# Optimization experiments

Hardware: AMD Instinct MI355X
Metric: run time of the kernel (lower is better)

## Reference

```python
import jax, jax.numpy as jnp
import numpy as np


def setup_inputs() -> dict:
    key = jax.random.key(0)
    k1, k2, k3, k4, k5 = jax.random.split(key, 5)
    B, T, H, E, F = 4, 2048, 2048, 8, 1024
    s_h = 1.0 / np.sqrt(H)
    s_f = 1.0 / np.sqrt(F)
    return {
        "hidden_states": jax.random.normal(k1, (B, T, H), dtype=jnp.float32),
        "W_router": jax.random.normal(k2, (H, E), dtype=jnp.float32) * s_h,
        "W_gate": jax.random.normal(k3, (E, H, F), dtype=jnp.float32) * s_h,
        "W_up": jax.random.normal(k4, (E, H, F), dtype=jnp.float32) * s_h,
        "W_down": jax.random.normal(k5, (E, F, H), dtype=jnp.float32) * s_f,
    }


def reference(hidden_states, W_router, W_gate, W_up, W_down):
    B, T, H = hidden_states.shape
    E = W_router.shape[1]
    x = hidden_states.reshape(-1, H)  # [N, H]
    # ReMoE router: linear -> ReLU, non-negative weights per expert
    weights = jax.nn.relu(x @ W_router)  # [N, E]
    # Per-expert SwiGLU FFN applied to all tokens; zero-weight experts
    # contribute exactly zero, matching the original masked dispatch.
    gate = jnp.einsum('nh,ehf->enf', x, W_gate)  # [E, N, F]
    up = jnp.einsum('nh,ehf->enf', x, W_up)      # [E, N, F]
    hid = jax.nn.silu(gate) * up                 # [E, N, F]
    expert_out = jnp.einsum('enf,efh->enh', hid, W_down)  # [E, N, H]
    out_flat = jnp.einsum('ne,enh->nh', weights, expert_out)  # [N, H]
    out = out_flat.reshape(B, T, H)
    router_weights = weights.reshape(B, T, E)
    return (out, router_weights)
```

## Files before the change

kernel.cpp:

```cpp
#include <hip/hip_runtime.h>
#include <hip/hip_bf16.h>

#define N_TOK 8192
#define HD    2048
#define NE    8
#define FF    1024

using f32x4  = __attribute__((ext_vector_type(4))) float;
using bf16x8 = __attribute__((ext_vector_type(8))) __bf16;

__device__ __forceinline__ unsigned short f2bf(float f) {
  unsigned u = __float_as_uint(f);
  u += 0x7FFFu + ((u >> 16) & 1u);
  return (unsigned short)(u >> 16);
}

__device__ __forceinline__ void gl_lds16(const void* g, void* l) {
  __builtin_amdgcn_global_load_lds((__attribute__((address_space(1))) void*)g,
                                   (__attribute__((address_space(3))) void*)l,
                                   16, 0, 0);
}

__device__ __forceinline__ void stage256(const unsigned short* g, size_t lda, int k0,
                                         char* slotbase, int wv, int sr8, int scol) {
  #pragma unroll
  for (int c = 0; c < 4; ++c) {
    const int grp = c * 8 + wv;
    gl_lds16(g + (size_t)(grp * 8 + sr8) * lda + k0 + scol, slotbase + grp * 1024);
  }
}
__device__ __forceinline__ void stage256i(const unsigned short* const aP[4], int k0,
                                          char* slotbase, int wv) {
  #pragma unroll
  for (int c = 0; c < 4; ++c) {
    const int grp = c * 8 + wv;
    gl_lds16(aP[c] + k0, slotbase + grp * 1024);
  }
}
__device__ __forceinline__ void stage128(const unsigned short* g, size_t lda, int k0,
                                         char* slotbase, int wv, int sr8, int scol) {
  #pragma unroll
  for (int c = 0; c < 2; ++c) {
    const int grp = c * 8 + wv;
    gl_lds16(g + (size_t)(grp * 8 + sr8) * lda + k0 + scol, slotbase + grp * 1024);
  }
}

__global__ void k_tconv(const float* __restrict__ in, unsigned short* __restrict__ out,
                        int R, int C, size_t in_z, size_t out_z, size_t ostride) {
  __shared__ float tile[32][33];
  const int z = blockIdx.z;
  const int c0 = blockIdx.x * 32, r0 = blockIdx.y * 32;
  const int tx = threadIdx.x, ty = threadIdx.y;
  const float* ip = in + (size_t)z * in_z;
  unsigned short* op = out + (size_t)z * out_z;
  #pragma unroll
  for (int i = ty; i < 32; i += 8)
    tile[i][tx] = ip[(size_t)(r0 + i) * C + (c0 + tx)];
  __syncthreads();
  #pragma unroll
  for (int i = ty; i < 32; i += 8)
    op[(size_t)(c0 + i) * ostride + (r0 + tx)] = f2bf(tile[tx][i]);
}

__global__ void k_router(const float* __restrict__ x, const float* __restrict__ Wr,
                         float* __restrict__ w, float* __restrict__ rout,
                         unsigned short* __restrict__ xb) {
  const int lane = threadIdx.x & 63, wv = threadIdx.x >> 6;
  const int n = blockIdx.x * 4 + wv;
  const float* xr = x + (size_t)n * HD + lane * 32;
  unsigned short* xbr = xb + (size_t)n * HD + lane * 32;
  const float* wbase = Wr + (size_t)lane * 32 * NE;
  float acc[8];
  #pragma unroll
  for (int e = 0; e < 8; ++e) acc[e] = 0.f;
  #pragma unroll
  for (int kk = 0; kk < 32; kk += 4) {
    float4 xv = *reinterpret_cast<const float4*>(xr + kk);
    ushort4 o;
    o.x = f2bf(xv.x); o.y = f2bf(xv.y); o.z = f2bf(xv.z); o.w = f2bf(xv.w);
    *reinterpret_cast<ushort4*>(xbr + kk) = o;
    #pragma unroll
    for (int t = 0; t < 4; ++t) {
      const float* wrow = wbase + (kk + t) * 8;
      float4 w0 = *reinterpret_cast<const float4*>(wrow);
      float4 w1 = *reinterpret_cast<const float4*>(wrow + 4);
      float xs = (t == 0) ? xv.x : (t == 1) ? xv.y : (t == 2) ? xv.z : xv.w;
      acc[0] += xs * w0.x; acc[1] += xs * w0.y; acc[2] += xs * w0.z; acc[3] += xs * w0.w;
      acc[4] += xs * w1.x; acc[5] += xs * w1.y; acc[6] += xs * w1.z; acc[7] += xs * w1.w;
    }
  }
  #pragma unroll
  for (int off = 32; off; off >>= 1) {
    #pragma unroll
    for (int e = 0; e < 8; ++e) acc[e] += __shfl_down(acc[e], off);
  }
  if (lane == 0) {
    #pragma unroll
    for (int e = 0; e < 8; ++e) {
      float v = acc[e] > 0.f ? acc[e] : 0.f;
      w[n * 8 + e] = v;
      rout[n * 8 + e] = v;
    }
  }
}

__global__ void k_compact(const float* __restrict__ w, int* __restrict__ idx,
                          int* __restrict__ rev, int* __restrict__ cnt) {
  const int e = blockIdx.x;
  __shared__ int base;
  __shared__ int scan[4];
  if (threadIdx.x == 0) base = 0;
  __syncthreads();
  const int lane = threadIdx.x & 63, wvi = threadIdx.x >> 6;
  for (int c0 = 0; c0 < N_TOK; c0 += 256) {
    const int n = c0 + threadIdx.x;
    const bool act = w[n * 8 + e] > 0.f;
    unsigned long long m = __ballot(act);
    const int pre  = __popcll(m & ((1ull << lane) - 1ull));
    if (lane == 0) scan[wvi] = __popcll(m);
    __syncthreads();
    int woff = 0;
    #pragma unroll
    for (int i = 0; i < 4; ++i) if (i < wvi) woff += scan[i];
    const int tot = scan[0] + scan[1] + scan[2] + scan[3];
    const int pos = base + woff + pre;
    if (act) idx[e * N_TOK + pos] = n;
    rev[n * NE + e] = act ? pos : -1;
    __syncthreads();
    if (threadIdx.x == 0) base += tot;
    __syncthreads();
  }
  const int M = base;
  if (threadIdx.x == 0) cnt[e] = M;
  const int Mpad = (M + 255) & ~255;
  for (int i = M + threadIdx.x; i < Mpad; i += 256) idx[e * N_TOK + i] = 0;
}

#define G1_PHASE(cpK) do {                                                       \
    const char* Ab_ = As + rs * 32768 + (wr * 64) * 128 + rb;                    \
    const char* Bg_ = Bgs + rs * 16384 + (wc * 64) * 128 + rb;                   \
    const char* Bu_ = Bus + rs * 16384 + (wc * 64) * 128 + rb;                   \
    bf16x8 av_[4], bg_[4], bu_[4];                                               \
    _Pragma("unroll")                                                            \
    for (int i = 0; i < 4; ++i) av_[i] = *(const bf16x8*)(Ab_ + i * 2048 + (cpK)); \
    _Pragma("unroll")                                                            \
    for (int j = 0; j < 4; ++j) {                                                \
      bg_[j] = *(const bf16x8*)(Bg_ + j * 2048 + (cpK));                         \
      bu_[j] = *(const bf16x8*)(Bu_ + j * 2048 + (cpK));                         \
    }                                                                            \
    __builtin_amdgcn_s_setprio(1);                                               \
    _Pragma("unroll")                                                            \
    for (int i = 0; i < 4; ++i) {                                                \
      _Pragma("unroll")                                                          \
      for (int j = 0; j < 4; ++j) {                                              \
        ag[i][j] = __builtin_amdgcn_mfma_f32_16x16x32_bf16(av_[i], bg_[j], ag[i][j], 0,0,0); \
        au[i][j] = __builtin_amdgcn_mfma_f32_16x16x32_bf16(av_[i], bu_[j], au[i][j], 0,0,0); \
      }                                                                          \
    }                                                                            \
    __builtin_amdgcn_s_setprio(0);                                               \
  } while (0)

__global__ void __launch_bounds__(512, 2) k_gemm1(
    const unsigned short* __restrict__ xb,
    const unsigned short* __restrict__ Wg,
    const unsigned short* __restrict__ Wu,
    const float* __restrict__ w,
    const int* __restrict__ idx,
    const int* __restrict__ cnt,
    unsigned short* __restrict__ A2,
    int e0, int k2g, int nwg, int compacted) {
  extern __shared__ char lds[];
  char* As  = lds;
  char* Bgs = lds + 65536;
  char* Bus = lds + 98304;
  const int tid = threadIdx.x;
  const int l = tid & 63, wv = tid >> 6;

  const int h = blockIdx.x;
  const int chunk = nwg >> 3;
  const int L = (h & 7) * chunk + (h >> 3);
  const int eloc = L >> 8;
  const int e = e0 + eloc;
  const int idxq = L & 255;
  const int sub = idxq >> 5;
  const int f = ((sub & 1) << 2) | ((idxq >> 3) & 3);
  const int y = ((sub >> 1) << 3) | (idxq & 7);
  const int bm = y << 8;
  const int bf = f << 7;
  const int wr = wv >> 1, wc = wv & 1;

  const int Me = cnt[e];
  if (bm >= Me) return;
  const int* idxe = idx + e * N_TOK;

  const unsigned short* gBg = Wg + ((size_t)e * FF + bf) * HD;
  const unsigned short* gBu = Wu + ((size_t)e * FF + bf) * HD;

  const int sr8  = l >> 3;
  const int scol = ((l & 7) ^ sr8) << 3;
  const int fr  = l & 15;
  const int rb  = fr << 7;
  const int kc  = (l >> 4) << 4;
  const int swz = (l & 7) << 4;
  const int cp0 = kc ^ swz;
  const int cp1 = (64 + kc) ^ swz;

  const unsigned short* aP[4];
  #pragma unroll
  for (int c = 0; c < 4; ++c)
    aP[c] = xb + (size_t)idxe[bm + (c * 8 + wv) * 8 + sr8] * HD + scol;

  f32x4 ag[4][4], au[4][4];
  const f32x4 zero = {0.f, 0.f, 0.f, 0.f};
  #pragma unroll
  for (int i = 0; i < 4; ++i) {
    #pragma unroll
    for (int j = 0; j < 4; ++j) { ag[i][j] = zero; au[i][j] = zero; }
  }

  stage256i(aP, 0, As, wv);
  stage128(gBg, HD, 0, Bgs, wv, sr8, scol);
  stage128(gBu, HD, 0, Bus, wv, sr8, scol);
  asm volatile("s_waitcnt vmcnt(0)" ::: "memory");
  __builtin_amdgcn_s_barrier();
  __builtin_amdgcn_sched_barrier(0);

  const int NT = HD / 64;
  for (int t = 0; t < NT; ++t) {
    const int tn = (t + 1 < NT) ? t + 1 : NT - 1;
    const int sw = (t + 1) & 1;
    const int rs = t & 1;
    stage128(gBg, HD, tn * 64, Bgs + sw * 16384, wv, sr8, scol);
    stage128(gBu, HD, tn * 64, Bus + sw * 16384, wv, sr8, scol);
    G1_PHASE(cp0);
    stage256i(aP, tn * 64, As + sw * 32768, wv);
    G1_PHASE(cp1);
    asm volatile("s_waitcnt vmcnt(0)" ::: "memory");
    __builtin_amdgcn_s_barrier();
    __builtin_amdgcn_sched_barrier(0);
  }

  const int orow = (l >> 4) << 2;
  #pragma unroll
  for (int am = 0; am < 4; ++am) {
    #pragma unroll
    for (int rr = 0; rr < 4; ++rr) {
      const int cm = bm + wr * 64 + am * 16 + orow + rr;
      const int n = idxe[cm];
      const float wn = w[n * 8 + e];
      size_t obase;
      if (compacted)
        obase = (size_t)eloc * N_TOK * FF + (size_t)cm * FF + bf + wc * 64 + fr;
      else
        obase = (size_t)n * k2g + (size_t)eloc * FF + bf + wc * 64 + fr;
      #pragma unroll
      for (int j = 0; j < 4; ++j) {
        const float g = ag[am][j][rr];
        const float u = au[am][j][rr];
        const float s = g / (1.f + __expf(-g));
        A2[obase + j * 16] = f2bf(s * u * wn);
      }
    }
  }
}

#define G2_PHASE(cpK) do {                                                       \
    const char* Ab_ = As + rs * 32768 + (wr * 128) * 128 + rb;                   \
    const char* Bb_ = Bs + rs * 32768 + (wc * 64) * 128 + rb;                    \
    bf16x8 av_[8], bv_[4];                                                       \
    _Pragma("unroll")                                                            \
    for (int i = 0; i < 8; ++i) av_[i] = *(const bf16x8*)(Ab_ + i * 2048 + (cpK)); \
    _Pragma("unroll")                                                            \
    for (int j = 0; j < 4; ++j) bv_[j] = *(const bf16x8*)(Bb_ + j * 2048 + (cpK)); \
    __builtin_amdgcn_s_setprio(1);                                               \
    _Pragma("unroll")                                                            \
    for (int i = 0; i < 8; ++i) {                                                \
      _Pragma("unroll")                                                          \
      for (int j = 0; j < 4; ++j)                                                \
        acc[i][j] = __builtin_amdgcn_mfma_f32_16x16x32_bf16(av_[i], bv_[j], acc[i][j], 0,0,0); \
    }                                                                            \
    __builtin_amdgcn_s_setprio(0);                                               \
  } while (0)

__global__ void __launch_bounds__(512, 2) k_gemm2(
    const unsigned short* __restrict__ A2,
    const unsigned short* __restrict__ Wd,
    float* __restrict__ out,
    int k2g, int accum) {
  extern __shared__ char lds[];
  char* As = lds;
  char* Bs = lds + 65536;
  const int tid = threadIdx.x;
  const int l = tid & 63, wv = tid >> 6;

  const int h = blockIdx.x;
  const int L = (h & 7) * 32 + (h >> 3);
  const int y = L >> 3;
  const int x = L & 7;
  const int bm = y << 8;
  const int bn = x << 8;
  const int wr = wv >> 2, wc = wv & 3;

  const unsigned short* gA = A2 + (size_t)bm * k2g;
  const unsigned short* gB = Wd + (size_t)bn * (NE * FF);

  const int sr8  = l >> 3;
  const int scol = ((l & 7) ^ sr8) << 3;
  const int fr  = l & 15;
  const int rb  = fr << 7;
  const int kc  = (l >> 4) << 4;
  const int swz = (l & 7) << 4;
  const int cp0 = kc ^ swz;
  const int cp1 = (64 + kc) ^ swz;

  f32x4 acc[8][4];
  const f32x4 zero = {0.f, 0.f, 0.f, 0.f};
  #pragma unroll
  for (int i = 0; i < 8; ++i) {
    #pragma unroll
    for (int j = 0; j < 4; ++j) acc[i][j] = zero;
  }

  stage256(gA, k2g, 0, As, wv, sr8, scol);
  stage256(gB, NE * FF, 0, Bs, wv, sr8, scol);
  asm volatile("s_waitcnt vmcnt(0)" ::: "memory");
  __builtin_amdgcn_s_barrier();
  __builtin_amdgcn_sched_barrier(0);

  const int NT = k2g / 64;
  for (int t = 0; t < NT; ++t) {
    const int tn = (t + 1 < NT) ? t + 1 : NT - 1;
    const int sw = (t + 1) & 1;
    const int rs = t & 1;
    stage256(gB, NE * FF, tn * 64, Bs + sw * 32768, wv, sr8, scol);
    G2_PHASE(cp0);
    stage256(gA, k2g, tn * 64, As + sw * 32768, wv, sr8, scol);
    G2_PHASE(cp1);
    asm volatile("s_waitcnt vmcnt(0)" ::: "memory");
    __builtin_amdgcn_s_barrier();
    __builtin_amdgcn_sched_barrier(0);
  }

  const int orow = (l >> 4) << 2;
  #pragma unroll
  for (int am = 0; am < 8; ++am) {
    #pragma unroll
    for (int rr = 0; rr < 4; ++rr) {
      const int n = bm + wr * 128 + am * 16 + orow + rr;
      float* op = out + (size_t)n * HD + bn + wc * 64 + fr;
      #pragma unroll
      for (int j = 0; j < 4; ++j) {
        const float v = acc[am][j][rr];
        op[j * 16] = accum ? (op[j * 16] + v) : v;
      }
    }
  }
}

__global__ void __launch_bounds__(512, 2) k_gemm2s(
    const unsigned short* __restrict__ A2c,
    const unsigned short* __restrict__ Wd,
    const int* __restrict__ cnt,
    float* __restrict__ outc) {
  extern __shared__ char lds[];
  char* As = lds;
  char* Bs = lds + 65536;
  const int tid = threadIdx.x;
  const int l = tid & 63, wv = tid >> 6;

  const int h = blockIdx.x;
  const int L = (h & 7) * 256 + (h >> 3);
  const int eloc = L >> 8;
  const int idxq = L & 255;
  const int x = idxq >> 5;
  const int y = idxq & 31;
  const int bm = y << 8;
  const int bn = x << 8;
  const int wr = wv >> 2, wc = wv & 3;

  const int Me = cnt[eloc];
  if (bm >= Me) return;

  const unsigned short* gA = A2c + (size_t)eloc * N_TOK * FF + (size_t)bm * FF;
  const unsigned short* gB = Wd + (size_t)bn * (NE * FF) + (size_t)eloc * FF;

  const int sr8  = l >> 3;
  const int scol = ((l & 7) ^ sr8) << 3;
  const int fr  = l & 15;
  const int rb  = fr << 7;
  const int kc  = (l >> 4) << 4;
  const int swz = (l & 7) << 4;
  const int cp0 = kc ^ swz;
  const int cp1 = (64 + kc) ^ swz;

  f32x4 acc[8][4];
  const f32x4 zero = {0.f, 0.f, 0.f, 0.f};
  #pragma unroll
  for (int i = 0; i < 8; ++i) {
    #pragma unroll
    for (int j = 0; j < 4; ++j) acc[i][j] = zero;
  }

  stage256(gA, FF, 0, As, wv, sr8, scol);
  stage256(gB, NE * FF, 0, Bs, wv, sr8, scol);
  asm volatile("s_waitcnt vmcnt(0)" ::: "memory");
  __builtin_amdgcn_s_barrier();
  __builtin_amdgcn_sched_barrier(0);

  const int NT = FF / 64;
  for (int t = 0; t < NT; ++t) {
    const int tn = (t + 1 < NT) ? t + 1 : NT - 1;
    const int sw = (t + 1) & 1;
    const int rs = t & 1;
    stage256(gB, NE * FF, tn * 64, Bs + sw * 32768, wv, sr8, scol);
    G2_PHASE(cp0);
    stage256(gA, FF, tn * 64, As + sw * 32768, wv, sr8, scol);
    G2_PHASE(cp1);
    asm volatile("s_waitcnt vmcnt(0)" ::: "memory");
    __builtin_amdgcn_s_barrier();
    __builtin_amdgcn_sched_barrier(0);
  }

  float* oce = outc + (size_t)eloc * N_TOK * HD;
  const int orow = (l >> 4) << 2;
  #pragma unroll
  for (int am = 0; am < 8; ++am) {
    #pragma unroll
    for (int rr = 0; rr < 4; ++rr) {
      const int cm = bm + wr * 128 + am * 16 + orow + rr;
      float* op = oce + (size_t)cm * HD + bn + wc * 64 + fr;
      #pragma unroll
      for (int j = 0; j < 4; ++j) op[j * 16] = acc[am][j][rr];
    }
  }
}

__global__ void k_gather(const float* __restrict__ outc, const int* __restrict__ rev,
                         float* __restrict__ out) {
  const int n = blockIdx.x;
  const int h0 = threadIdx.x * 8;
  float4 a0 = {0.f, 0.f, 0.f, 0.f}, a1 = {0.f, 0.f, 0.f, 0.f};
  #pragma unroll
  for (int e = 0; e < NE; ++e) {
    const int cm = rev[n * NE + e];
    if (cm >= 0) {
      const float4* p = reinterpret_cast<const float4*>(
          outc + (size_t)e * N_TOK * HD + (size_t)cm * HD + h0);
      float4 v0 = p[0], v1 = p[1];
      a0.x += v0.x; a0.y += v0.y; a0.z += v0.z; a0.w += v0.w;
      a1.x += v1.x; a1.y += v1.y; a1.z += v1.z; a1.w += v1.w;
    }
  }
  float4* op = reinterpret_cast<float4*>(out + (size_t)n * HD + h0);
  op[0] = a0; op[1] = a1;
}

extern "C" void kernel_launch(void* const* d_in, const int* in_sizes, int n_in,
                              void* d_out, int out_size, void* d_ws, size_t ws_size,
                              hipStream_t stream) {
  (void)in_sizes; (void)out_size;
  if (n_in < 5) return;
  const float* x  = (const float*)d_in[0];
  const float* Wr = (const float*)d_in[1];
  const float* Wg = (const float*)d_in[2];
  const float* Wu = (const float*)d_in[3];
  const float* Wd = (const float*)d_in[4];
  float* out  = (float*)d_out;
  float* rout = out + (size_t)N_TOK * HD;

  hipFuncSetAttribute((const void*)k_gemm1,  hipFuncAttributeMaxDynamicSharedMemorySize, 131072);
  hipFuncSetAttribute((const void*)k_gemm2,  hipFuncAttributeMaxDynamicSharedMemorySize, 131072);
  hipFuncSetAttribute((const void*)k_gemm2s, hipFuncAttributeMaxDynamicSharedMemorySize, 131072);

  char* ws = (char*)d_ws;
  const size_t SZ_XB = (size_t)N_TOK * HD * 2;
  const size_t SZ_W  = (size_t)NE * HD * FF * 2;
  unsigned short* xb    = (unsigned short*)(ws);
  unsigned short* Wg_bt = (unsigned short*)(ws + SZ_XB);
  unsigned short* Wu_bt = (unsigned short*)(ws + SZ_XB + SZ_W);
  unsigned short* Wd_bt = (unsigned short*)(ws + SZ_XB + 2 * SZ_W);
  float*          wbuf  = (float*)(ws + SZ_XB + 3 * SZ_W);
  size_t off = SZ_XB + 3 * SZ_W + (size_t)N_TOK * NE * 4;
  int* idxbuf = (int*)(ws + off);  off += (size_t)NE * N_TOK * 4;
  int* revbuf = (int*)(ws + off);  off += (size_t)NE * N_TOK * 4;
  int* cntbuf = (int*)(ws + off);  off += 256;
  const size_t fixed = off;
  unsigned short* A2 = (unsigned short*)(ws + fixed);

  const size_t perE = (size_t)N_TOK * FF * 2;
  const size_t SZ_A2   = (size_t)NE * perE;
  const size_t SZ_OUTC = (size_t)NE * N_TOK * HD * 4;
  float* outc = (float*)(ws + fixed + SZ_A2);

  const bool sparse2 = (ws_size >= fixed + SZ_A2 + SZ_OUTC);

  dim3 tb(32, 8);
  k_tconv<<<dim3(FF / 32, HD / 32, NE), tb, 0, stream>>>(
      Wg, Wg_bt, HD, FF, (size_t)HD * FF, (size_t)FF * HD, (size_t)HD);
  k_tconv<<<dim3(FF / 32, HD / 32, NE), tb, 0, stream>>>(
      Wu, Wu_bt, HD, FF, (size_t)HD * FF, (size_t)FF * HD, (size_t)HD);
  k_tconv<<<dim3(HD / 32, FF / 32, NE), tb, 0, stream>>>(
      Wd, Wd_bt, FF, HD, (size_t)FF * HD, (size_t)FF, (size_t)(NE * FF));

  k_router<<<N_TOK / 4, 256, 0, stream>>>(x, Wr, wbuf, rout, xb);

  k_compact<<<NE, 256, 0, stream>>>(wbuf, idxbuf, revbuf, cntbuf);

  if (sparse2) {
    const int nwg1 = 256 * NE;
    k_gemm1<<<nwg1, 512, 131072, stream>>>(xb, Wg_bt, Wu_bt, wbuf, idxbuf, cntbuf,
                                           A2, 0, NE * FF, nwg1, 1);
    k_gemm2s<<<2048, 512, 131072, stream>>>(A2, Wd_bt, cntbuf, outc);
    k_gather<<<N_TOK, 256, 0, stream>>>(outc, revbuf, out);
  } else {
    int G = 8;
    while (G > 1 && fixed + (size_t)G * perE > ws_size) G >>= 1;
    const int k2g = G * FF;
    for (int e0 = 0; e0 < NE; e0 += G) {
      hipMemsetAsync(A2, 0, (size_t)G * perE, stream);
      const int nwg1 = 256 * G;
      k_gemm1<<<nwg1, 512, 131072, stream>>>(xb, Wg_bt, Wu_bt, wbuf, idxbuf, cntbuf,
                                             A2, e0, k2g, nwg1, 0);
      k_gemm2<<<(N_TOK / 256) * (HD / 256), 512, 131072, stream>>>(
          A2, Wd_bt + (size_t)e0 * FF, out, k2g, e0 != 0);
    }
  }
}
```

Measured before the change: 699.3 us.

## Store per-expert down-proj outputs in bf16 and group experts to fit workspace

The sparse down-projection kernel now writes its per-expert output buffer as bf16 instead of fp32. The gather kernel reads bf16, widens to fp32 and can accumulate across several expert groups. The host picks the largest expert group size whose A2 and output buffers fit in the workspace, and loops over groups, so the sparse path is usable with less workspace. The aim is to halve the write and read traffic of the intermediate expert outputs. The cost is an extra bf16 rounding of each expert's output before the weighted sum, and extra launches when the group is smaller than all experts.

```diff
diff --git a/kernel.cpp b/kernel.cpp
--- a/kernel.cpp
+++ b/kernel.cpp
@@ -8,6 +8,7 @@
 
 using f32x4  = __attribute__((ext_vector_type(4))) float;
 using bf16x8 = __attribute__((ext_vector_type(8))) __bf16;
+using u16x8  = __attribute__((ext_vector_type(8))) unsigned short;
 
 __device__ __forceinline__ unsigned short f2bf(float f) {
   unsigned u = __float_as_uint(f);
@@ -362,7 +363,8 @@
     const unsigned short* __restrict__ A2c,
     const unsigned short* __restrict__ Wd,
     const int* __restrict__ cnt,
-    float* __restrict__ outc) {
+    unsigned short* __restrict__ outc,
+    int e0, int nwg) {
   extern __shared__ char lds[];
   char* As = lds;
   char* Bs = lds + 65536;
@@ -370,8 +372,10 @@
   const int l = tid & 63, wv = tid >> 6;
 
   const int h = blockIdx.x;
-  const int L = (h & 7) * 256 + (h >> 3);
+  const int chunk = nwg >> 3;
+  const int L = (h & 7) * chunk + (h >> 3);
   const int eloc = L >> 8;
+  const int e = e0 + eloc;
   const int idxq = L & 255;
   const int x = idxq >> 5;
   const int y = idxq & 31;
@@ -379,11 +383,11 @@
   const int bn = x << 8;
   const int wr = wv >> 2, wc = wv & 3;
 
-  const int Me = cnt[eloc];
+  const int Me = cnt[e];
   if (bm >= Me) return;
 
   const unsigned short* gA = A2c + (size_t)eloc * N_TOK * FF + (size_t)bm * FF;
-  const unsigned short* gB = Wd + (size_t)bn * (NE * FF) + (size_t)eloc * FF;
+  const unsigned short* gB = Wd + (size_t)bn * (NE * FF) + (size_t)e * FF;
 
   const int sr8  = l >> 3;
   const int scol = ((l & 7) ^ sr8) << 3;
@@ -422,38 +426,51 @@
     __builtin_amdgcn_sched_barrier(0);
   }
 
-  float* oce = outc + (size_t)eloc * N_TOK * HD;
+  unsigned short* oce = outc + (size_t)eloc * N_TOK * HD;
   const int orow = (l >> 4) << 2;
   #pragma unroll
   for (int am = 0; am < 8; ++am) {
     #pragma unroll
     for (int rr = 0; rr < 4; ++rr) {
       const int cm = bm + wr * 128 + am * 16 + orow + rr;
-      float* op = oce + (size_t)cm * HD + bn + wc * 64 + fr;
+      unsigned short* op = oce + (size_t)cm * HD + bn + wc * 64 + fr;
       #pragma unroll
-      for (int j = 0; j < 4; ++j) op[j * 16] = acc[am][j][rr];
-    }
-  }
-}
-
-__global__ void k_gather(const float* __restrict__ outc, const int* __restrict__ rev,
-                         float* __restrict__ out) {
+      for (int j = 0; j < 4; ++j) op[j * 16] = f2bf(acc[am][j][rr]);
+    }
+  }
+}
+
+__global__ void k_gather(const unsigned short* __restrict__ outc,
+                         const int* __restrict__ rev,
+                         float* __restrict__ out,
+                         int e0, int G, int accum) {
   const int n = blockIdx.x;
   const int h0 = threadIdx.x * 8;
-  float4 a0 = {0.f, 0.f, 0.f, 0.f}, a1 = {0.f, 0.f, 0.f, 0.f};
-  #pragma unroll
-  for (int e = 0; e < NE; ++e) {
-    const int cm = rev[n * NE + e];
+  float* op = out + (size_t)n * HD + h0;
+  float a[8];
+  if (accum) {
+    float4 v0 = reinterpret_cast<const float4*>(op)[0];
+    float4 v1 = reinterpret_cast<const float4*>(op)[1];
+    a[0] = v0.x; a[1] = v0.y; a[2] = v0.z; a[3] = v0.w;
+    a[4] = v1.x; a[5] = v1.y; a[6] = v1.z; a[7] = v1.w;
+  } else {
+    #pragma unroll
+    for (int i = 0; i < 8; ++i) a[i] = 0.f;
+  }
+  for (int g = 0; g < G; ++g) {
+    const int cm = rev[n * NE + (e0 + g)];
     if (cm >= 0) {
-      const float4* p = reinterpret_cast<const float4*>(
-          outc + (size_t)e * N_TOK * HD + (size_t)cm * HD + h0);
-      float4 v0 = p[0], v1 = p[1];
-      a0.x += v0.x; a0.y += v0.y; a0.z += v0.z; a0.w += v0.w;
-      a1.x += v1.x; a1.y += v1.y; a1.z += v1.z; a1.w += v1.w;
-    }
-  }
-  float4* op = reinterpret_cast<float4*>(out + (size_t)n * HD + h0);
-  op[0] = a0; op[1] = a1;
+      u16x8 v = *reinterpret_cast<const u16x8*>(
+          outc + (size_t)g * N_TOK * HD + (size_t)cm * HD + h0);
+      #pragma unroll
+      for (int i = 0; i < 8; ++i)
+        a[i] += __uint_as_float(((unsigned)v[i]) << 16);
+    }
+  }
+  float4 o0 = {a[0], a[1], a[2], a[3]};
+  float4 o1 = {a[4], a[5], a[6], a[7]};
+  reinterpret_cast<float4*>(op)[0] = o0;
+  reinterpret_cast<float4*>(op)[1] = o1;
 }
 
 extern "C" void kernel_launch(void* const* d_in, const int* in_sizes, int n_in,
@@ -486,14 +503,13 @@
   int* revbuf = (int*)(ws + off);  off += (size_t)NE * N_TOK * 4;
   int* cntbuf = (int*)(ws + off);  off += 256;
   const size_t fixed = off;
-  unsigned short* A2 = (unsigned short*)(ws + fixed);
-
-  const size_t perE = (size_t)N_TOK * FF * 2;
-  const size_t SZ_A2   = (size_t)NE * perE;
-  const size_t SZ_OUTC = (size_t)NE * N_TOK * HD * 4;
-  float* outc = (float*)(ws + fixed + SZ_A2);
-
-  const bool sparse2 = (ws_size >= fixed + SZ_A2 + SZ_OUTC);
+
+  const size_t perE   = (size_t)N_TOK * FF * 2;
+  const size_t perEoc = (size_t)N_TOK * HD * 2;
+
+  int Gs = 0;
+  for (int g = NE; g >= 2; g >>= 1)
+    if (fixed + (size_t)g * (perE + perEoc) <= ws_size) { Gs = g; break; }
 
   dim3 tb(32, 8);
   k_tconv<<<dim3(FF / 32, HD / 32, NE), tb, 0, stream>>>(
@@ -507,13 +523,18 @@
 
   k_compact<<<NE, 256, 0, stream>>>(wbuf, idxbuf, revbuf, cntbuf);
 
-  if (sparse2) {
-    const int nwg1 = 256 * NE;
-    k_gemm1<<<nwg1, 512, 131072, stream>>>(xb, Wg_bt, Wu_bt, wbuf, idxbuf, cntbuf,
-                                           A2, 0, NE * FF, nwg1, 1);
-    k_gemm2s<<<2048, 512, 131072, stream>>>(A2, Wd_bt, cntbuf, outc);
-    k_gather<<<N_TOK, 256, 0, stream>>>(outc, revbuf, out);
+  if (Gs >= 2) {
+    unsigned short* A2c  = (unsigned short*)(ws + fixed);
+    unsigned short* outc = (unsigned short*)(ws + fixed + (size_t)Gs * perE);
+    for (int e0 = 0; e0 < NE; e0 += Gs) {
+      const int nwg = 256 * Gs;
+      k_gemm1<<<nwg, 512, 131072, stream>>>(xb, Wg_bt, Wu_bt, wbuf, idxbuf, cntbuf,
+                                            A2c, e0, 0, nwg, 1);
+      k_gemm2s<<<nwg, 512, 131072, stream>>>(A2c, Wd_bt, cntbuf, outc, e0, nwg);
+      k_gather<<<N_TOK, 256, 0, stream>>>(outc, revbuf, out, e0, Gs, e0 != 0);
+    }
   } else {
+    unsigned short* A2 = (unsigned short*)(ws + fixed);
     int G = 8;
     while (G > 1 && fixed + (size_t)G * perE > ws_size) G >>= 1;
     const int k2g = G * FF;
```

Result: slower. 928.3 us (+32.7%).
